# Kernel optimization log

Hardware: AMD Instinct MI355X
Metric: run time of the kernel (lower is better)

Reference implementation:

```python
import jax, jax.numpy as jnp
import numpy as np


def _lstm(x, w_ih, w_hh, b_ih, b_hh):
    # x: [B, T, D]; w_ih: [4H, D]; w_hh: [4H, H]. PyTorch gate order: i, f, g, o.
    B, T, D = x.shape
    H = w_hh.shape[1]
    # Precompute input contributions for all timesteps: [B, T, 4H]
    xg = jnp.einsum('btd,gd->btg', x, w_ih) + b_ih + b_hh
    xg = jnp.transpose(xg, (1, 0, 2))  # [T, B, 4H]

    def step(carry, xt):
        h, c = carry
        gates = xt + h @ w_hh.T  # [B, 4H]
        i, f, g, o = jnp.split(gates, 4, axis=-1)
        i = jax.nn.sigmoid(i)
        f = jax.nn.sigmoid(f)
        g = jnp.tanh(g)
        o = jax.nn.sigmoid(o)
        c = f * c + i * g
        h = o * jnp.tanh(c)
        return (h, c), h

    h0 = jnp.zeros((B, H), dtype=x.dtype)
    c0 = jnp.zeros((B, H), dtype=x.dtype)
    (_, _), hs = jax.lax.scan(step, (h0, c0), xg)
    return jnp.transpose(hs, (1, 0, 2))  # [B, T, H]


def setup_inputs() -> dict:
    key = jax.random.key(0)
    ks = jax.random.split(key, 11)
    B, T, D, H1, H2, OUT = 2048, 128, 128, 128, 64, 64
    s1 = 1.0 / np.sqrt(H1)
    s2 = 1.0 / np.sqrt(H2)
    return {
        'x': jax.random.normal(ks[0], (B, T, D), dtype=jnp.float32),
        'w_ih1': jax.random.uniform(ks[1], (4 * H1, D), jnp.float32, -s1, s1),
        'w_hh1': jax.random.uniform(ks[2], (4 * H1, H1), jnp.float32, -s1, s1),
        'b_ih1': jax.random.uniform(ks[3], (4 * H1,), jnp.float32, -s1, s1),
        'b_hh1': jax.random.uniform(ks[4], (4 * H1,), jnp.float32, -s1, s1),
        'w_ih2': jax.random.uniform(ks[5], (4 * H2, H1), jnp.float32, -s2, s2),
        'w_hh2': jax.random.uniform(ks[6], (4 * H2, H2), jnp.float32, -s2, s2),
        'b_ih2': jax.random.uniform(ks[7], (4 * H2,), jnp.float32, -s2, s2),
        'b_hh2': jax.random.uniform(ks[8], (4 * H2,), jnp.float32, -s2, s2),
        'w_dense': jax.random.uniform(ks[9], (OUT, H2), jnp.float32, -s2, s2),
        'b_dense': jax.random.uniform(ks[10], (OUT,), jnp.float32, -s2, s2),
    }


def reference(x, w_ih1, w_hh1, b_ih1, b_hh1, w_ih2, w_hh2, b_ih2, b_hh2, w_dense, b_dense):
    # Dropout is identity in eval mode.
    h = _lstm(x, w_ih1, w_hh1, b_ih1, b_hh1)          # [B, T, H1]
    h = _lstm(h, w_ih2, w_hh2, b_ih2, b_hh2)          # [B, T, H2]
    last = h[:, -1, :]                                 # [B, H2]
    return jax.nn.relu(last @ w_dense.T + b_dense)     # [B, 64]
```

## Files before the change

kernel.cpp:

```cpp
#include <hip/hip_runtime.h>
#include <hip/hip_bf16.h>

#define BB  2048
#define TT  128
#define DD  128
#define HH1 128
#define GG1 512
#define HH2 64
#define GG2 256
#define OO  64

typedef __attribute__((ext_vector_type(8))) short  short8;
typedef __attribute__((ext_vector_type(4))) float  floatx4;

#define PIN(x) asm volatile("" : "+v"(x))

#define OFF_WHH1 0
#define OFF_WIH1 131072
#define OFF_WIH2 262144
#define OFF_WHH2 327680
#define OFF_B1   360448
#define OFF_B2   362496
#define OFF_XBF  524288
#define OFF_H1S  67633152

__device__ __forceinline__ short f2bf(float f) {
  unsigned u = __float_as_uint(f);
  unsigned r = (u + 0x7FFFu + ((u >> 16) & 1u)) >> 16;
  return (short)r;
}
__device__ __forceinline__ float sigm(float x) {
  return __builtin_amdgcn_rcpf(1.0f + __expf(-x));
}
__device__ __forceinline__ float tanh_fast(float x) {
  return 1.0f - 2.0f * __builtin_amdgcn_rcpf(1.0f + __expf(2.0f * x));
}

__device__ __forceinline__ void lds_barrier() {
  asm volatile("s_waitcnt lgkmcnt(0)" ::: "memory");
  __builtin_amdgcn_s_barrier();
  asm volatile("" ::: "memory");
}

__global__ void k_prep(const float* __restrict__ wih1, const float* __restrict__ whh1,
                       const float* __restrict__ bih1, const float* __restrict__ bhh1,
                       const float* __restrict__ wih2, const float* __restrict__ whh2,
                       const float* __restrict__ bih2, const float* __restrict__ bhh2,
                       char* __restrict__ ws) {
  short* WHH1 = (short*)(ws + OFF_WHH1);
  short* WIH1 = (short*)(ws + OFF_WIH1);
  short* WIH2 = (short*)(ws + OFF_WIH2);
  short* WHH2 = (short*)(ws + OFF_WHH2);
  float* B1 = (float*)(ws + OFF_B1);
  float* B2 = (float*)(ws + OFF_B2);
  int idx = blockIdx.x * blockDim.x + threadIdx.x;
  int stride = gridDim.x * blockDim.x;
  for (int i = idx; i < GG1 * DD; i += stride) { WIH1[i] = f2bf(wih1[i]); WHH1[i] = f2bf(whh1[i]); }
  for (int i = idx; i < GG2 * HH1; i += stride) WIH2[i] = f2bf(wih2[i]);
  for (int i = idx; i < GG2 * HH2; i += stride) WHH2[i] = f2bf(whh2[i]);
  for (int i = idx; i < GG1; i += stride) B1[i] = bih1[i] + bhh1[i];
  for (int i = idx; i < GG2; i += stride) B2[i] = bih2[i] + bhh2[i];
}

__global__ __launch_bounds__(256) void k_xcast(const float* __restrict__ x,
                                               short* __restrict__ xbf) {
  size_t i = ((size_t)blockIdx.x * 256 + threadIdx.x) * 8;
  float4 a = *(const float4*)&x[i];
  float4 b = *(const float4*)&x[i + 4];
  short8 o;
  o[0] = f2bf(a.x); o[1] = f2bf(a.y); o[2] = f2bf(a.z); o[3] = f2bf(a.w);
  o[4] = f2bf(b.x); o[5] = f2bf(b.y); o[6] = f2bf(b.z); o[7] = f2bf(b.w);
  *(short8*)&xbf[i] = o;
}

__global__ __launch_bounds__(512, 2) void k_rec1f(const char* __restrict__ ws,
                                                  short* __restrict__ h1s) {
  __shared__ short hbds[2][16 * 136];
  const short* WHH = (const short*)(ws + OFF_WHH1);
  const short* WIH = (const short*)(ws + OFF_WIH1);
  const short* XBF = (const short*)(ws + OFF_XBF);
  const float* B1 = (const float*)(ws + OFF_B1);
  const int lane = threadIdx.x & 63;
  const int wv = threadIdx.x >> 6;
  const int col = lane & 15, quad = lane >> 4;
  const int hc = wv * 16 + col;
  const int r0 = blockIdx.x * 8;

  short8 wh[4][4], wx[4][4];
#pragma unroll
  for (int gt = 0; gt < 4; ++gt)
#pragma unroll
    for (int kk = 0; kk < 4; ++kk) {
      wh[gt][kk] = *(const short8*)&WHH[(gt * 128 + hc) * HH1 + kk * 32 + quad * 8];
      wx[gt][kk] = *(const short8*)&WIH[(gt * 128 + hc) * DD + kk * 32 + quad * 8];
      PIN(wh[gt][kk]);
      PIN(wx[gt][kk]);
    }
  float bias[4];
#pragma unroll
  for (int gt = 0; gt < 4; ++gt) bias[gt] = B1[gt * 128 + hc];

  for (int i = threadIdx.x; i < 2 * 16 * 136; i += 512) ((short*)hbds)[i] = 0;

  const bool aload = (col < 8);
  const short* xbase = XBF + (size_t)(r0 + (col & 7)) * TT * DD;
  const short8 zz = {0, 0, 0, 0, 0, 0, 0, 0};
  short8 ax_cur[4], ax_nxt[4];

  floatx4 accA[4], accB[4];
  {
    short8 ax0[4];
#pragma unroll
    for (int kk = 0; kk < 4; ++kk)
      ax0[kk] = aload ? *(const short8*)&xbase[kk * 32 + quad * 8] : zz;
#pragma unroll
    for (int gt = 0; gt < 4; ++gt)
      accA[gt] = (floatx4){bias[gt], bias[gt], bias[gt], bias[gt]};
#pragma unroll
    for (int kk = 0; kk < 4; ++kk)
#pragma unroll
      for (int gt = 0; gt < 4; ++gt)
        accA[gt] = __builtin_amdgcn_mfma_f32_16x16x32_bf16(ax0[kk], wx[gt][kk], accA[gt], 0, 0, 0);
  }
#pragma unroll
  for (int kk = 0; kk < 4; ++kk) {
    ax_cur[kk] = aload ? *(const short8*)&xbase[DD + kk * 32 + quad * 8] : zz;
    ax_nxt[kk] = ax_cur[kk];
  }

  const int row0 = (quad & 1) * 4 + (quad >> 1) * 2;
  float c0 = 0.f, c1 = 0.f;
  __syncthreads();

  auto step = [&](int t, short* rbuf, short* wbuf, floatx4* A, floatx4* Bn) {
    if (aload && t + 2 < TT) {
#pragma unroll
      for (int kk = 0; kk < 4; ++kk)
        ax_nxt[kk] = *(const short8*)&xbase[(t + 2) * DD + kk * 32 + quad * 8];
    }
    short8 ah[4];
#pragma unroll
    for (int kk = 0; kk < 4; ++kk)
      ah[kk] = *(const short8*)&rbuf[col * 136 + kk * 32 + quad * 8];
#pragma unroll
    for (int kk = 0; kk < 4; ++kk)
#pragma unroll
      for (int gt = 0; gt < 4; ++gt)
        A[gt] = __builtin_amdgcn_mfma_f32_16x16x32_bf16(ah[kk], wh[gt][kk], A[gt], 0, 0, 0);
#pragma unroll
    for (int gt = 0; gt < 4; ++gt)
      Bn[gt] = (floatx4){bias[gt], bias[gt], bias[gt], bias[gt]};
#pragma unroll
    for (int kk = 0; kk < 4; ++kk)
#pragma unroll
      for (int gt = 0; gt < 4; ++gt)
        Bn[gt] = __builtin_amdgcn_mfma_f32_16x16x32_bf16(ax_cur[kk], wx[gt][kk], Bn[gt], 0, 0, 0);

    float g0[4], g1[4];
#pragma unroll
    for (int gt = 0; gt < 4; ++gt) {
      float v2 = __shfl_xor(A[gt][2], 32);
      float v3 = __shfl_xor(A[gt][3], 32);
      g0[gt] = (quad < 2) ? A[gt][0] : v2;
      g1[gt] = (quad < 2) ? A[gt][1] : v3;
    }
    {
      float i0 = sigm(g0[0]), f0 = sigm(g0[1]), gg0 = tanh_fast(g0[2]), o0 = sigm(g0[3]);
      c0 = fmaf(f0, c0, i0 * gg0);
      float hA = o0 * tanh_fast(c0);
      float i1 = sigm(g1[0]), f1 = sigm(g1[1]), gg1 = tanh_fast(g1[2]), o1 = sigm(g1[3]);
      c1 = fmaf(f1, c1, i1 * gg1);
      float hB = o1 * tanh_fast(c1);
      short ha = f2bf(hA), hbv = f2bf(hB);
      wbuf[(row0)     * 136 + hc] = ha;
      wbuf[(row0 + 1) * 136 + hc] = hbv;
      h1s[((size_t)(r0 + row0)     * TT + t) * HH1 + hc] = ha;
      h1s[((size_t)(r0 + row0 + 1) * TT + t) * HH1 + hc] = hbv;
    }
    lds_barrier();
#pragma unroll
    for (int kk = 0; kk < 4; ++kk) ax_cur[kk] = ax_nxt[kk];
  };

  for (int t = 0; t < TT; t += 2) {
    step(t,     &hbds[0][0], &hbds[1][0], accA, accB);
    step(t + 1, &hbds[1][0], &hbds[0][0], accB, accA);
  }
}

__global__ __launch_bounds__(512, 2) void k_rec2f(const char* __restrict__ ws,
                                                  const short* __restrict__ h1s,
                                                  const float* __restrict__ wd,
                                                  const float* __restrict__ bd,
                                                  float* __restrict__ out) {
  __shared__ short hbuf[16 * 72];
  __shared__ float gsm[8 * 260];
  __shared__ float h2f[8 * HH2];
  const short* WHH = (const short*)(ws + OFF_WHH2);
  const short* WIH = (const short*)(ws + OFF_WIH2);
  const float* B2 = (const float*)(ws + OFF_B2);
  const int lane = threadIdx.x & 63;
  const int wv = threadIdx.x >> 6;
  const int col = lane & 15, quad = lane >> 4;
  const int n0 = wv * 32;
  const int r0 = blockIdx.x * 8;

  short8 wh[2][2], wx[2][4];
#pragma unroll
  for (int nt = 0; nt < 2; ++nt) {
#pragma unroll
    for (int kk = 0; kk < 2; ++kk) {
      wh[nt][kk] = *(const short8*)&WHH[(n0 + nt * 16 + col) * HH2 + kk * 32 + quad * 8];
      PIN(wh[nt][kk]);
    }
#pragma unroll
    for (int kk = 0; kk < 4; ++kk) {
      wx[nt][kk] = *(const short8*)&WIH[(n0 + nt * 16 + col) * HH1 + kk * 32 + quad * 8];
      PIN(wx[nt][kk]);
    }
  }
  float bias[2];
#pragma unroll
  for (int nt = 0; nt < 2; ++nt) bias[nt] = B2[n0 + nt * 16 + col];

  for (int i = threadIdx.x; i < 16 * 72; i += 512) hbuf[i] = 0;

  const bool aload = (col < 8);
  const short* h1base = h1s + (size_t)(r0 + (col & 7)) * TT * HH1;
  const short8 zz = {0, 0, 0, 0, 0, 0, 0, 0};
  short8 ax_cur[4], ax_nxt[4];

  floatx4 accA[2], accB[2];
  {
    short8 ax0[4];
#pragma unroll
    for (int kk = 0; kk < 4; ++kk)
      ax0[kk] = aload ? *(const short8*)&h1base[kk * 32 + quad * 8] : zz;
#pragma unroll
    for (int nt = 0; nt < 2; ++nt)
      accA[nt] = (floatx4){bias[nt], bias[nt], bias[nt], bias[nt]};
#pragma unroll
    for (int kk = 0; kk < 4; ++kk)
#pragma unroll
      for (int nt = 0; nt < 2; ++nt)
        accA[nt] = __builtin_amdgcn_mfma_f32_16x16x32_bf16(ax0[kk], wx[nt][kk], accA[nt], 0, 0, 0);
  }
#pragma unroll
  for (int kk = 0; kk < 4; ++kk) {
    ax_cur[kk] = aload ? *(const short8*)&h1base[HH1 + kk * 32 + quad * 8] : zz;
    ax_nxt[kk] = ax_cur[kk];
  }

  const int j = threadIdx.x & 63;
  const int rr = threadIdx.x >> 6;
  float cc = 0.f;
  __syncthreads();

  auto step = [&](int t, floatx4* A, floatx4* Bn) {
    short8 ah[2];
#pragma unroll
    for (int kk = 0; kk < 2; ++kk)
      ah[kk] = *(const short8*)&hbuf[col * 72 + kk * 32 + quad * 8];
#pragma unroll
    for (int kk = 0; kk < 2; ++kk)
#pragma unroll
      for (int nt = 0; nt < 2; ++nt)
        A[nt] = __builtin_amdgcn_mfma_f32_16x16x32_bf16(ah[kk], wh[nt][kk], A[nt], 0, 0, 0);

    if (quad < 2) {
#pragma unroll
      for (int nt = 0; nt < 2; ++nt)
#pragma unroll
        for (int r = 0; r < 4; ++r)
          gsm[(quad * 4 + r) * 260 + n0 + nt * 16 + col] = A[nt][r];
    }

#pragma unroll
    for (int nt = 0; nt < 2; ++nt)
      Bn[nt] = (floatx4){bias[nt], bias[nt], bias[nt], bias[nt]};
#pragma unroll
    for (int kk = 0; kk < 4; ++kk)
#pragma unroll
      for (int nt = 0; nt < 2; ++nt)
        Bn[nt] = __builtin_amdgcn_mfma_f32_16x16x32_bf16(ax_cur[kk], wx[nt][kk], Bn[nt], 0, 0, 0);
    if (aload && t + 2 < TT) {
#pragma unroll
      for (int kk = 0; kk < 4; ++kk)
        ax_nxt[kk] = *(const short8*)&h1base[(t + 2) * HH1 + kk * 32 + quad * 8];
    }

    lds_barrier();

    {
      float i0 = gsm[rr * 260 + j],       f0 = gsm[rr * 260 + 64 + j];
      float g0 = gsm[rr * 260 + 128 + j], o0 = gsm[rr * 260 + 192 + j];
      cc = fmaf(sigm(f0), cc, sigm(i0) * tanh_fast(g0));
      float hh = sigm(o0) * tanh_fast(cc);
      hbuf[rr * 72 + j] = f2bf(hh);
      if (t == TT - 1) h2f[rr * HH2 + j] = hh;
    }
    lds_barrier();
#pragma unroll
    for (int kk = 0; kk < 4; ++kk) ax_cur[kk] = ax_nxt[kk];
  };

  for (int t = 0; t < TT; t += 2) {
    step(t,     accA, accB);
    step(t + 1, accB, accA);
  }

  {
    const int o = threadIdx.x & 63;
    const int r = threadIdx.x >> 6;
    float acc = bd[o];
    for (int k = 0; k < HH2; ++k)
      acc = fmaf(h2f[r * HH2 + k], wd[o * HH2 + k], acc);
    out[(size_t)(r0 + r) * OO + o] = fmaxf(acc, 0.f);
  }
}

extern "C" void kernel_launch(void* const* d_in, const int* in_sizes, int n_in,
                              void* d_out, int out_size, void* d_ws, size_t ws_size,
                              hipStream_t stream) {
  const float* x       = (const float*)d_in[0];
  const float* w_ih1   = (const float*)d_in[1];
  const float* w_hh1   = (const float*)d_in[2];
  const float* b_ih1   = (const float*)d_in[3];
  const float* b_hh1   = (const float*)d_in[4];
  const float* w_ih2   = (const float*)d_in[5];
  const float* w_hh2   = (const float*)d_in[6];
  const float* b_ih2   = (const float*)d_in[7];
  const float* b_hh2   = (const float*)d_in[8];
  const float* w_dense = (const float*)d_in[9];
  const float* b_dense = (const float*)d_in[10];
  char* ws = (char*)d_ws;
  short* xbf = (short*)(ws + OFF_XBF);
  short* h1s = (short*)(ws + OFF_H1S);
  float* out = (float*)d_out;

  hipLaunchKernelGGL(k_prep, dim3(256), dim3(256), 0, stream,
                     w_ih1, w_hh1, b_ih1, b_hh1, w_ih2, w_hh2, b_ih2, b_hh2, ws);
  hipLaunchKernelGGL(k_xcast, dim3((BB * TT * DD) / (256 * 8)), dim3(256), 0, stream, x, xbf);
  hipLaunchKernelGGL(k_rec1f, dim3(BB / 8), dim3(512), 0, stream, ws, h1s);
  hipLaunchKernelGGL(k_rec2f, dim3(BB / 8), dim3(512), 0, stream, ws, h1s, w_dense, b_dense, out);
}
```

Measured before the change: 424.6 us.

## Prescale gate weights for exp2 activations and restructure layer-2 recurrence

```diff
diff --git a/kernel.cpp b/kernel.cpp
--- a/kernel.cpp
+++ b/kernel.cpp
@@ -24,16 +24,22 @@
 #define OFF_XBF  524288
 #define OFF_H1S  67633152
 
+#define L2E      1.44269504088896340736f
+#define TWO_L2E  2.88539008177792681472f
+
 __device__ __forceinline__ short f2bf(float f) {
   unsigned u = __float_as_uint(f);
   unsigned r = (u + 0x7FFFu + ((u >> 16) & 1u)) >> 16;
   return (short)r;
 }
-__device__ __forceinline__ float sigm(float x) {
-  return __builtin_amdgcn_rcpf(1.0f + __expf(-x));
-}
-__device__ __forceinline__ float tanh_fast(float x) {
-  return 1.0f - 2.0f * __builtin_amdgcn_rcpf(1.0f + __expf(2.0f * x));
+__device__ __forceinline__ float exp2_f(float x) {
+  float r; asm("v_exp_f32 %0, %1" : "=v"(r) : "v"(x)); return r;
+}
+__device__ __forceinline__ float sigm2(float y) {
+  return __builtin_amdgcn_rcpf(1.0f + exp2_f(y));
+}
+__device__ __forceinline__ float tanh2(float y) {
+  return fmaf(-2.0f, __builtin_amdgcn_rcpf(1.0f + exp2_f(y)), 1.0f);
 }
 
 __device__ __forceinline__ void lds_barrier() {
@@ -55,11 +61,28 @@
   float* B2 = (float*)(ws + OFF_B2);
   int idx = blockIdx.x * blockDim.x + threadIdx.x;
   int stride = gridDim.x * blockDim.x;
-  for (int i = idx; i < GG1 * DD; i += stride) { WIH1[i] = f2bf(wih1[i]); WHH1[i] = f2bf(whh1[i]); }
-  for (int i = idx; i < GG2 * HH1; i += stride) WIH2[i] = f2bf(wih2[i]);
-  for (int i = idx; i < GG2 * HH2; i += stride) WHH2[i] = f2bf(whh2[i]);
-  for (int i = idx; i < GG1; i += stride) B1[i] = bih1[i] + bhh1[i];
-  for (int i = idx; i < GG2; i += stride) B2[i] = bih2[i] + bhh2[i];
+  const float SCI = -L2E, SCG = TWO_L2E;
+  for (int i = idx; i < GG1 * DD; i += stride) {
+    int g = (i >> 7) >> 7;
+    float s = (g == 2) ? SCG : SCI;
+    WIH1[i] = f2bf(wih1[i] * s); WHH1[i] = f2bf(whh1[i] * s);
+  }
+  for (int i = idx; i < GG2 * HH1; i += stride) {
+    int g = (i >> 7) >> 6; float s = (g == 2) ? SCG : SCI;
+    WIH2[i] = f2bf(wih2[i] * s);
+  }
+  for (int i = idx; i < GG2 * HH2; i += stride) {
+    int g = (i >> 6) >> 6; float s = (g == 2) ? SCG : SCI;
+    WHH2[i] = f2bf(whh2[i] * s);
+  }
+  for (int i = idx; i < GG1; i += stride) {
+    float s = ((i >> 7) == 2) ? SCG : SCI;
+    B1[i] = (bih1[i] + bhh1[i]) * s;
+  }
+  for (int i = idx; i < GG2; i += stride) {
+    float s = ((i >> 6) == 2) ? SCG : SCI;
+    B2[i] = (bih2[i] + bhh2[i]) * s;
+  }
 }
 
 __global__ __launch_bounds__(256) void k_xcast(const float* __restrict__ x,
@@ -96,18 +119,22 @@
       PIN(wh[gt][kk]);
       PIN(wx[gt][kk]);
     }
-  float bias[4];
-#pragma unroll
-  for (int gt = 0; gt < 4; ++gt) bias[gt] = B1[gt * 128 + hc];
+  floatx4 BIASV[4];
+#pragma unroll
+  for (int gt = 0; gt < 4; ++gt) {
+    float b = B1[gt * 128 + hc];
+    BIASV[gt] = (floatx4){b, b, b, b};
+    PIN(BIASV[gt]);
+  }
 
   for (int i = threadIdx.x; i < 2 * 16 * 136; i += 512) ((short*)hbds)[i] = 0;
 
   const bool aload = (col < 8);
   const short* xbase = XBF + (size_t)(r0 + (col & 7)) * TT * DD;
   const short8 zz = {0, 0, 0, 0, 0, 0, 0, 0};
-  short8 ax_cur[4], ax_nxt[4];
-
+  short8 axA[4], axB[4];
   floatx4 accA[4], accB[4];
+
   {
     short8 ax0[4];
 #pragma unroll
@@ -115,28 +142,29 @@
       ax0[kk] = aload ? *(const short8*)&xbase[kk * 32 + quad * 8] : zz;
 #pragma unroll
     for (int gt = 0; gt < 4; ++gt)
-      accA[gt] = (floatx4){bias[gt], bias[gt], bias[gt], bias[gt]};
-#pragma unroll
-    for (int kk = 0; kk < 4; ++kk)
+      accA[gt] = __builtin_amdgcn_mfma_f32_16x16x32_bf16(ax0[0], wx[gt][0], BIASV[gt], 0, 0, 0);
+#pragma unroll
+    for (int kk = 1; kk < 4; ++kk)
 #pragma unroll
       for (int gt = 0; gt < 4; ++gt)
         accA[gt] = __builtin_amdgcn_mfma_f32_16x16x32_bf16(ax0[kk], wx[gt][kk], accA[gt], 0, 0, 0);
   }
 #pragma unroll
   for (int kk = 0; kk < 4; ++kk) {
-    ax_cur[kk] = aload ? *(const short8*)&xbase[DD + kk * 32 + quad * 8] : zz;
-    ax_nxt[kk] = ax_cur[kk];
+    axA[kk] = aload ? *(const short8*)&xbase[DD + kk * 32 + quad * 8] : zz;
+    axB[kk] = zz;
   }
 
   const int row0 = (quad & 1) * 4 + (quad >> 1) * 2;
   float c0 = 0.f, c1 = 0.f;
   __syncthreads();
 
-  auto step = [&](int t, short* rbuf, short* wbuf, floatx4* A, floatx4* Bn) {
+  auto step = [&](int t, short* rbuf, short* wbuf, floatx4* A, floatx4* Bn,
+                  short8* axC, short8* axP) {
     if (aload && t + 2 < TT) {
 #pragma unroll
       for (int kk = 0; kk < 4; ++kk)
-        ax_nxt[kk] = *(const short8*)&xbase[(t + 2) * DD + kk * 32 + quad * 8];
+        axP[kk] = *(const short8*)&xbase[(t + 2) * DD + kk * 32 + quad * 8];
     }
     short8 ah[4];
 #pragma unroll
@@ -149,12 +177,12 @@
         A[gt] = __builtin_amdgcn_mfma_f32_16x16x32_bf16(ah[kk], wh[gt][kk], A[gt], 0, 0, 0);
 #pragma unroll
     for (int gt = 0; gt < 4; ++gt)
-      Bn[gt] = (floatx4){bias[gt], bias[gt], bias[gt], bias[gt]};
-#pragma unroll
-    for (int kk = 0; kk < 4; ++kk)
-#pragma unroll
-      for (int gt = 0; gt < 4; ++gt)
-        Bn[gt] = __builtin_amdgcn_mfma_f32_16x16x32_bf16(ax_cur[kk], wx[gt][kk], Bn[gt], 0, 0, 0);
+      Bn[gt] = __builtin_amdgcn_mfma_f32_16x16x32_bf16(axC[0], wx[gt][0], BIASV[gt], 0, 0, 0);
+#pragma unroll
+    for (int kk = 1; kk < 4; ++kk)
+#pragma unroll
+      for (int gt = 0; gt < 4; ++gt)
+        Bn[gt] = __builtin_amdgcn_mfma_f32_16x16x32_bf16(axC[kk], wx[gt][kk], Bn[gt], 0, 0, 0);
 
     float g0[4], g1[4];
 #pragma unroll
@@ -165,12 +193,12 @@
       g1[gt] = (quad < 2) ? A[gt][1] : v3;
     }
     {
-      float i0 = sigm(g0[0]), f0 = sigm(g0[1]), gg0 = tanh_fast(g0[2]), o0 = sigm(g0[3]);
+      float i0 = sigm2(g0[0]), f0 = sigm2(g0[1]), gg0 = tanh2(g0[2]), o0 = sigm2(g0[3]);
       c0 = fmaf(f0, c0, i0 * gg0);
-      float hA = o0 * tanh_fast(c0);
-      float i1 = sigm(g1[0]), f1 = sigm(g1[1]), gg1 = tanh_fast(g1[2]), o1 = sigm(g1[3]);
+      float hA = o0 * tanh2(c0 * TWO_L2E);
+      float i1 = sigm2(g1[0]), f1 = sigm2(g1[1]), gg1 = tanh2(g1[2]), o1 = sigm2(g1[3]);
       c1 = fmaf(f1, c1, i1 * gg1);
-      float hB = o1 * tanh_fast(c1);
+      float hB = o1 * tanh2(c1 * TWO_L2E);
       short ha = f2bf(hA), hbv = f2bf(hB);
       wbuf[(row0)     * 136 + hc] = ha;
       wbuf[(row0 + 1) * 136 + hc] = hbv;
@@ -178,135 +206,140 @@
       h1s[((size_t)(r0 + row0 + 1) * TT + t) * HH1 + hc] = hbv;
     }
     lds_barrier();
-#pragma unroll
-    for (int kk = 0; kk < 4; ++kk) ax_cur[kk] = ax_nxt[kk];
   };
 
   for (int t = 0; t < TT; t += 2) {
-    step(t,     &hbds[0][0], &hbds[1][0], accA, accB);
-    step(t + 1, &hbds[1][0], &hbds[0][0], accB, accA);
-  }
-}
-
-__global__ __launch_bounds__(512, 2) void k_rec2f(const char* __restrict__ ws,
+    step(t,     &hbds[0][0], &hbds[1][0], accA, accB, axA, axB);
+    step(t + 1, &hbds[1][0], &hbds[0][0], accB, accA, axB, axA);
+  }
+}
+
+__global__ __launch_bounds__(256, 2) void k_rec2r(const char* __restrict__ ws,
                                                   const short* __restrict__ h1s,
                                                   const float* __restrict__ wd,
                                                   const float* __restrict__ bd,
                                                   float* __restrict__ out) {
-  __shared__ short hbuf[16 * 72];
-  __shared__ float gsm[8 * 260];
-  __shared__ float h2f[8 * HH2];
+  __shared__ short hbds[2][16 * 72];
+  __shared__ float h2f[4 * HH2];
   const short* WHH = (const short*)(ws + OFF_WHH2);
   const short* WIH = (const short*)(ws + OFF_WIH2);
   const float* B2 = (const float*)(ws + OFF_B2);
   const int lane = threadIdx.x & 63;
   const int wv = threadIdx.x >> 6;
   const int col = lane & 15, quad = lane >> 4;
-  const int n0 = wv * 32;
-  const int r0 = blockIdx.x * 8;
-
-  short8 wh[2][2], wx[2][4];
-#pragma unroll
-  for (int nt = 0; nt < 2; ++nt) {
+  const int hc = wv * 16 + col;
+  const int r0 = blockIdx.x * 4;
+
+  short8 wh[4][2], wx[4][4];
+#pragma unroll
+  for (int gt = 0; gt < 4; ++gt) {
 #pragma unroll
     for (int kk = 0; kk < 2; ++kk) {
-      wh[nt][kk] = *(const short8*)&WHH[(n0 + nt * 16 + col) * HH2 + kk * 32 + quad * 8];
-      PIN(wh[nt][kk]);
+      wh[gt][kk] = *(const short8*)&WHH[(gt * 64 + hc) * HH2 + kk * 32 + quad * 8];
+      PIN(wh[gt][kk]);
     }
 #pragma unroll
     for (int kk = 0; kk < 4; ++kk) {
-      wx[nt][kk] = *(const short8*)&WIH[(n0 + nt * 16 + col) * HH1 + kk * 32 + quad * 8];
-      PIN(wx[nt][kk]);
-    }
-  }
-  float bias[2];
-#pragma unroll
-  for (int nt = 0; nt < 2; ++nt) bias[nt] = B2[n0 + nt * 16 + col];
-
-  for (int i = threadIdx.x; i < 16 * 72; i += 512) hbuf[i] = 0;
-
-  const bool aload = (col < 8);
-  const short* h1base = h1s + (size_t)(r0 + (col & 7)) * TT * HH1;
+      wx[gt][kk] = *(const short8*)&WIH[(gt * 64 + hc) * HH1 + kk * 32 + quad * 8];
+      PIN(wx[gt][kk]);
+    }
+  }
+  floatx4 BIASV[4];
+#pragma unroll
+  for (int gt = 0; gt < 4; ++gt) {
+    float b = B2[gt * 64 + hc];
+    BIASV[gt] = (floatx4){b, b, b, b};
+    PIN(BIASV[gt]);
+  }
+
+  for (int i = threadIdx.x; i < 2 * 16 * 72; i += 256) ((short*)hbds)[i] = 0;
+
+  const bool aload = (col < 4);
+  const short* h1base = h1s + (size_t)(r0 + (col & 3)) * TT * HH1;
   const short8 zz = {0, 0, 0, 0, 0, 0, 0, 0};
-  short8 ax_cur[4], ax_nxt[4];
-
-  floatx4 accA[2], accB[2];
+  short8 axA[4], axB[4];
+  floatx4 accA[4], accB[4];
+
   {
     short8 ax0[4];
 #pragma unroll
     for (int kk = 0; kk < 4; ++kk)
       ax0[kk] = aload ? *(const short8*)&h1base[kk * 32 + quad * 8] : zz;
 #pragma unroll
-    for (int nt = 0; nt < 2; ++nt)
-      accA[nt] = (floatx4){bias[nt], bias[nt], bias[nt], bias[nt]};
-#pragma unroll
-    for (int kk = 0; kk < 4; ++kk)
-#pragma unroll
-      for (int nt = 0; nt < 2; ++nt)
-        accA[nt] = __builtin_amdgcn_mfma_f32_16x16x32_bf16(ax0[kk], wx[nt][kk], accA[nt], 0, 0, 0);
+    for (int gt = 0; gt < 4; ++gt)
+      accA[gt] = __builtin_amdgcn_mfma_f32_16x16x32_bf16(ax0[0], wx[gt][0], BIASV[gt], 0, 0, 0);
+#pragma unroll
+    for (int kk = 1; kk < 4; ++kk)
+#pragma unroll
+      for (int gt = 0; gt < 4; ++gt)
+        accA[gt] = __builtin_amdgcn_mfma_f32_16x16x32_bf16(ax0[kk], wx[gt][kk], accA[gt], 0, 0, 0);
   }
 #pragma unroll
   for (int kk = 0; kk < 4; ++kk) {
-    ax_cur[kk] = aload ? *(const short8*)&h1base[HH1 + kk * 32 + quad * 8] : zz;
-    ax_nxt[kk] = ax_cur[kk];
-  }
-
-  const int j = threadIdx.x & 63;
-  const int rr = threadIdx.x >> 6;
-  float cc = 0.f;
+    axA[kk] = aload ? *(const short8*)&h1base[HH1 + kk * 32 + quad * 8] : zz;
+    axB[kk] = zz;
+  }
+
+  const int row0 = (quad & 1) * 4 + (quad >> 1) * 2;
+  const bool realq = ((quad & 1) == 0);
+  float c0 = 0.f, c1 = 0.f;
   __syncthreads();
 
-  auto step = [&](int t, floatx4* A, floatx4* Bn) {
+  auto step = [&](int t, short* rbuf, short* wbuf, floatx4* A, floatx4* Bn,
+                  short8* axC, short8* axP) {
+    if (aload && t + 2 < TT) {
+#pragma unroll
+      for (int kk = 0; kk < 4; ++kk)
+        axP[kk] = *(const short8*)&h1base[(t + 2) * HH1 + kk * 32 + quad * 8];
+    }
     short8 ah[2];
 #pragma unroll
     for (int kk = 0; kk < 2; ++kk)
-      ah[kk] = *(const short8*)&hbuf[col * 72 + kk * 32 + quad * 8];
+      ah[kk] = *(const short8*)&rbuf[col * 72 + kk * 32 + quad * 8];
 #pragma unroll
     for (int kk = 0; kk < 2; ++kk)
 #pragma unroll
-      for (int nt = 0; nt < 2; ++nt)
-        A[nt] = __builtin_amdgcn_mfma_f32_16x16x32_bf16(ah[kk], wh[nt][kk], A[nt], 0, 0, 0);
-
-    if (quad < 2) {
-#pragma unroll
-      for (int nt = 0; nt < 2; ++nt)
-#pragma unroll
-        for (int r = 0; r < 4; ++r)
-          gsm[(quad * 4 + r) * 260 + n0 + nt * 16 + col] = A[nt][r];
-    }
-
-#pragma unroll
-    for (int nt = 0; nt < 2; ++nt)
-      Bn[nt] = (floatx4){bias[nt], bias[nt], bias[nt], bias[nt]};
-#pragma unroll
-    for (int kk = 0; kk < 4; ++kk)
-#pragma unroll
-      for (int nt = 0; nt < 2; ++nt)
-        Bn[nt] = __builtin_amdgcn_mfma_f32_16x16x32_bf16(ax_cur[kk], wx[nt][kk], Bn[nt], 0, 0, 0);
-    if (aload && t + 2 < TT) {
-#pragma unroll
-      for (int kk = 0; kk < 4; ++kk)
-        ax_nxt[kk] = *(const short8*)&h1base[(t + 2) * HH1 + kk * 32 + quad * 8];
-    }
-
+      for (int gt = 0; gt < 4; ++gt)
+        A[gt] = __builtin_amdgcn_mfma_f32_16x16x32_bf16(ah[kk], wh[gt][kk], A[gt], 0, 0, 0);
+#pragma unroll
+    for (int gt = 0; gt < 4; ++gt)
+      Bn[gt] = __builtin_amdgcn_mfma_f32_16x16x32_bf16(axC[0], wx[gt][0], BIASV[gt], 0, 0, 0);
+#pragma unroll
+    for (int kk = 1; kk < 4; ++kk)
+#pragma unroll
+      for (int gt = 0; gt < 4; ++gt)
+        Bn[gt] = __builtin_amdgcn_mfma_f32_16x16x32_bf16(axC[kk], wx[gt][kk], Bn[gt], 0, 0, 0);
+
+    float g0[4], g1[4];
+#pragma unroll
+    for (int gt = 0; gt < 4; ++gt) {
+      float v2 = __shfl_xor(A[gt][2], 32);
+      float v3 = __shfl_xor(A[gt][3], 32);
+      g0[gt] = (quad < 2) ? A[gt][0] : v2;
+      g1[gt] = (quad < 2) ? A[gt][1] : v3;
+    }
+    {
+      float i0 = sigm2(g0[0]), f0 = sigm2(g0[1]), gg0 = tanh2(g0[2]), o0 = sigm2(g0[3]);
+      c0 = fmaf(f0, c0, i0 * gg0);
+      float hA = o0 * tanh2(c0 * TWO_L2E);
+      float i1 = sigm2(g1[0]), f1 = sigm2(g1[1]), gg1 = tanh2(g1[2]), o1 = sigm2(g1[3]);
+      c1 = fmaf(f1, c1, i1 * gg1);
+      float hB = o1 * tanh2(c1 * TWO_L2E);
+      if (realq) {
+        wbuf[(row0)     * 72 + hc] = f2bf(hA);
+        wbuf[(row0 + 1) * 72 + hc] = f2bf(hB);
+        if (t == TT - 1) {
+          h2f[(row0)     * HH2 + hc] = hA;
+          h2f[(row0 + 1) * HH2 + hc] = hB;
+        }
+      }
+    }
     lds_barrier();
-
-    {
-      float i0 = gsm[rr * 260 + j],       f0 = gsm[rr * 260 + 64 + j];
-      float g0 = gsm[rr * 260 + 128 + j], o0 = gsm[rr * 260 + 192 + j];
-      cc = fmaf(sigm(f0), cc, sigm(i0) * tanh_fast(g0));
-      float hh = sigm(o0) * tanh_fast(cc);
-      hbuf[rr * 72 + j] = f2bf(hh);
-      if (t == TT - 1) h2f[rr * HH2 + j] = hh;
-    }
-    lds_barrier();
-#pragma unroll
-    for (int kk = 0; kk < 4; ++kk) ax_cur[kk] = ax_nxt[kk];
   };
 
   for (int t = 0; t < TT; t += 2) {
-    step(t,     accA, accB);
-    step(t + 1, accB, accA);
+    step(t,     &hbds[0][0], &hbds[1][0], accA, accB, axA, axB);
+    step(t + 1, &hbds[1][0], &hbds[0][0], accB, accA, axB, axA);
   }
 
   {
@@ -342,5 +375,5 @@
                      w_ih1, w_hh1, b_ih1, b_hh1, w_ih2, w_hh2, b_ih2, b_hh2, ws);
   hipLaunchKernelGGL(k_xcast, dim3((BB * TT * DD) / (256 * 8)), dim3(256), 0, stream, x, xbf);
   hipLaunchKernelGGL(k_rec1f, dim3(BB / 8), dim3(512), 0, stream, ws, h1s);
-  hipLaunchKernelGGL(k_rec2f, dim3(BB / 8), dim3(512), 0, stream, ws, h1s, w_dense, b_dense, out);
-}
+  hipLaunchKernelGGL(k_rec2r, dim3(BB / 4), dim3(256), 0, stream, ws, h1s, w_dense, b_dense, out);
+}
```

Measured after the change: 446.5 us. 1.05x slower.

## Fuse x bf16 cast into layer-1 recurrence and prescale gate weights for exp2

Applied to the files above, without the earlier changes.

```diff
diff --git a/kernel.cpp b/kernel.cpp
--- a/kernel.cpp
+++ b/kernel.cpp
@@ -21,19 +21,29 @@
 #define OFF_WHH2 327680
 #define OFF_B1   360448
 #define OFF_B2   362496
-#define OFF_XBF  524288
 #define OFF_H1S  67633152
+
+#define L2E      1.44269504088896340736f
+#define TWO_L2E  2.88539008177792681472f
 
 __device__ __forceinline__ short f2bf(float f) {
   unsigned u = __float_as_uint(f);
   unsigned r = (u + 0x7FFFu + ((u >> 16) & 1u)) >> 16;
   return (short)r;
 }
-__device__ __forceinline__ float sigm(float x) {
-  return __builtin_amdgcn_rcpf(1.0f + __expf(-x));
-}
-__device__ __forceinline__ float tanh_fast(float x) {
-  return 1.0f - 2.0f * __builtin_amdgcn_rcpf(1.0f + __expf(2.0f * x));
+__device__ __forceinline__ float exp2_f(float x) {
+  float r; asm("v_exp_f32 %0, %1" : "=v"(r) : "v"(x)); return r;
+}
+__device__ __forceinline__ float sigm2(float y) {
+  return __builtin_amdgcn_rcpf(1.0f + exp2_f(y));
+}
+__device__ __forceinline__ float tanh2(float y) {
+  return fmaf(-2.0f, __builtin_amdgcn_rcpf(1.0f + exp2_f(y)), 1.0f);
+}
+__device__ __forceinline__ unsigned cvtpk(float a, float b) {
+  unsigned r;
+  asm("v_cvt_pk_bf16_f32 %0, %1, %2" : "=v"(r) : "v"(a), "v"(b));
+  return r;
 }
 
 __device__ __forceinline__ void lds_barrier() {
@@ -55,30 +65,36 @@
   float* B2 = (float*)(ws + OFF_B2);
   int idx = blockIdx.x * blockDim.x + threadIdx.x;
   int stride = gridDim.x * blockDim.x;
-  for (int i = idx; i < GG1 * DD; i += stride) { WIH1[i] = f2bf(wih1[i]); WHH1[i] = f2bf(whh1[i]); }
-  for (int i = idx; i < GG2 * HH1; i += stride) WIH2[i] = f2bf(wih2[i]);
-  for (int i = idx; i < GG2 * HH2; i += stride) WHH2[i] = f2bf(whh2[i]);
-  for (int i = idx; i < GG1; i += stride) B1[i] = bih1[i] + bhh1[i];
-  for (int i = idx; i < GG2; i += stride) B2[i] = bih2[i] + bhh2[i];
-}
-
-__global__ __launch_bounds__(256) void k_xcast(const float* __restrict__ x,
-                                               short* __restrict__ xbf) {
-  size_t i = ((size_t)blockIdx.x * 256 + threadIdx.x) * 8;
-  float4 a = *(const float4*)&x[i];
-  float4 b = *(const float4*)&x[i + 4];
-  short8 o;
-  o[0] = f2bf(a.x); o[1] = f2bf(a.y); o[2] = f2bf(a.z); o[3] = f2bf(a.w);
-  o[4] = f2bf(b.x); o[5] = f2bf(b.y); o[6] = f2bf(b.z); o[7] = f2bf(b.w);
-  *(short8*)&xbf[i] = o;
+  const float SCI = -L2E, SCG = TWO_L2E;
+  for (int i = idx; i < GG1 * DD; i += stride) {
+    int g = (i >> 7) >> 7;
+    float s = (g == 2) ? SCG : SCI;
+    WIH1[i] = f2bf(wih1[i] * s); WHH1[i] = f2bf(whh1[i] * s);
+  }
+  for (int i = idx; i < GG2 * HH1; i += stride) {
+    int g = (i >> 7) >> 6; float s = (g == 2) ? SCG : SCI;
+    WIH2[i] = f2bf(wih2[i] * s);
+  }
+  for (int i = idx; i < GG2 * HH2; i += stride) {
+    int g = (i >> 6) >> 6; float s = (g == 2) ? SCG : SCI;
+    WHH2[i] = f2bf(whh2[i] * s);
+  }
+  for (int i = idx; i < GG1; i += stride) {
+    float s = ((i >> 7) == 2) ? SCG : SCI;
+    B1[i] = (bih1[i] + bhh1[i]) * s;
+  }
+  for (int i = idx; i < GG2; i += stride) {
+    float s = ((i >> 6) == 2) ? SCG : SCI;
+    B2[i] = (bih2[i] + bhh2[i]) * s;
+  }
 }
 
 __global__ __launch_bounds__(512, 2) void k_rec1f(const char* __restrict__ ws,
+                                                  const float* __restrict__ x,
                                                   short* __restrict__ h1s) {
   __shared__ short hbds[2][16 * 136];
   const short* WHH = (const short*)(ws + OFF_WHH1);
   const short* WIH = (const short*)(ws + OFF_WIH1);
-  const short* XBF = (const short*)(ws + OFF_XBF);
   const float* B1 = (const float*)(ws + OFF_B1);
   const int lane = threadIdx.x & 63;
   const int wv = threadIdx.x >> 6;
@@ -96,36 +112,48 @@
       PIN(wh[gt][kk]);
       PIN(wx[gt][kk]);
     }
-  float bias[4];
-#pragma unroll
-  for (int gt = 0; gt < 4; ++gt) bias[gt] = B1[gt * 128 + hc];
+  floatx4 BIASV[4];
+#pragma unroll
+  for (int gt = 0; gt < 4; ++gt) {
+    float b = B1[gt * 128 + hc];
+    BIASV[gt] = (floatx4){b, b, b, b};
+    PIN(BIASV[gt]);
+  }
 
   for (int i = threadIdx.x; i < 2 * 16 * 136; i += 512) ((short*)hbds)[i] = 0;
 
   const bool aload = (col < 8);
-  const short* xbase = XBF + (size_t)(r0 + (col & 7)) * TT * DD;
-  const short8 zz = {0, 0, 0, 0, 0, 0, 0, 0};
-  short8 ax_cur[4], ax_nxt[4];
+  const float* xbase = x + (size_t)(r0 + (col & 7)) * TT * DD;
+  float4 xf[4][2];
+#pragma unroll
+  for (int kk = 0; kk < 4; ++kk) {
+    xf[kk][0] = (float4){0.f, 0.f, 0.f, 0.f};
+    xf[kk][1] = (float4){0.f, 0.f, 0.f, 0.f};
+  }
 
   floatx4 accA[4], accB[4];
   {
     short8 ax0[4];
 #pragma unroll
-    for (int kk = 0; kk < 4; ++kk)
-      ax0[kk] = aload ? *(const short8*)&xbase[kk * 32 + quad * 8] : zz;
+    for (int kk = 0; kk < 4; ++kk) {
+      float4 f0 = (float4){0.f, 0.f, 0.f, 0.f}, f1 = f0;
+      if (aload) {
+        f0 = *(const float4*)&xbase[kk * 32 + quad * 8];
+        f1 = *(const float4*)&xbase[kk * 32 + quad * 8 + 4];
+      }
+      union { unsigned u[4]; short8 s; } cv;
+      cv.u[0] = cvtpk(f0.x, f0.y); cv.u[1] = cvtpk(f0.z, f0.w);
+      cv.u[2] = cvtpk(f1.x, f1.y); cv.u[3] = cvtpk(f1.z, f1.w);
+      ax0[kk] = cv.s;
+    }
 #pragma unroll
     for (int gt = 0; gt < 4; ++gt)
-      accA[gt] = (floatx4){bias[gt], bias[gt], bias[gt], bias[gt]};
-#pragma unroll
-    for (int kk = 0; kk < 4; ++kk)
+      accA[gt] = __builtin_amdgcn_mfma_f32_16x16x32_bf16(ax0[0], wx[gt][0], BIASV[gt], 0, 0, 0);
+#pragma unroll
+    for (int kk = 1; kk < 4; ++kk)
 #pragma unroll
       for (int gt = 0; gt < 4; ++gt)
         accA[gt] = __builtin_amdgcn_mfma_f32_16x16x32_bf16(ax0[kk], wx[gt][kk], accA[gt], 0, 0, 0);
-  }
-#pragma unroll
-  for (int kk = 0; kk < 4; ++kk) {
-    ax_cur[kk] = aload ? *(const short8*)&xbase[DD + kk * 32 + quad * 8] : zz;
-    ax_nxt[kk] = ax_cur[kk];
   }
 
   const int row0 = (quad & 1) * 4 + (quad >> 1) * 2;
@@ -133,10 +161,13 @@
   __syncthreads();
 
   auto step = [&](int t, short* rbuf, short* wbuf, floatx4* A, floatx4* Bn) {
-    if (aload && t + 2 < TT) {
-#pragma unroll
-      for (int kk = 0; kk < 4; ++kk)
-        ax_nxt[kk] = *(const short8*)&xbase[(t + 2) * DD + kk * 32 + quad * 8];
+    const bool doNext = (t + 1 < TT);
+    if (aload && doNext) {
+#pragma unroll
+      for (int kk = 0; kk < 4; ++kk) {
+        xf[kk][0] = *(const float4*)&xbase[(t + 1) * DD + kk * 32 + quad * 8];
+        xf[kk][1] = *(const float4*)&xbase[(t + 1) * DD + kk * 32 + quad * 8 + 4];
+      }
     }
     short8 ah[4];
 #pragma unroll
@@ -147,14 +178,26 @@
 #pragma unroll
       for (int gt = 0; gt < 4; ++gt)
         A[gt] = __builtin_amdgcn_mfma_f32_16x16x32_bf16(ah[kk], wh[gt][kk], A[gt], 0, 0, 0);
-#pragma unroll
-    for (int gt = 0; gt < 4; ++gt)
-      Bn[gt] = (floatx4){bias[gt], bias[gt], bias[gt], bias[gt]};
-#pragma unroll
-    for (int kk = 0; kk < 4; ++kk)
+    if (doNext) {
+      short8 axn[4];
+#pragma unroll
+      for (int kk = 0; kk < 4; ++kk) {
+        union { unsigned u[4]; short8 s; } cv;
+        cv.u[0] = cvtpk(xf[kk][0].x, xf[kk][0].y);
+        cv.u[1] = cvtpk(xf[kk][0].z, xf[kk][0].w);
+        cv.u[2] = cvtpk(xf[kk][1].x, xf[kk][1].y);
+        cv.u[3] = cvtpk(xf[kk][1].z, xf[kk][1].w);
+        axn[kk] = cv.s;
+      }
 #pragma unroll
       for (int gt = 0; gt < 4; ++gt)
-        Bn[gt] = __builtin_amdgcn_mfma_f32_16x16x32_bf16(ax_cur[kk], wx[gt][kk], Bn[gt], 0, 0, 0);
+        Bn[gt] = __builtin_amdgcn_mfma_f32_16x16x32_bf16(axn[0], wx[gt][0], BIASV[gt], 0, 0, 0);
+#pragma unroll
+      for (int kk = 1; kk < 4; ++kk)
+#pragma unroll
+        for (int gt = 0; gt < 4; ++gt)
+          Bn[gt] = __builtin_amdgcn_mfma_f32_16x16x32_bf16(axn[kk], wx[gt][kk], Bn[gt], 0, 0, 0);
+    }
 
     float g0[4], g1[4];
 #pragma unroll
@@ -165,12 +208,12 @@
       g1[gt] = (quad < 2) ? A[gt][1] : v3;
     }
     {
-      float i0 = sigm(g0[0]), f0 = sigm(g0[1]), gg0 = tanh_fast(g0[2]), o0 = sigm(g0[3]);
+      float i0 = sigm2(g0[0]), f0 = sigm2(g0[1]), gg0 = tanh2(g0[2]), o0 = sigm2(g0[3]);
       c0 = fmaf(f0, c0, i0 * gg0);
-      float hA = o0 * tanh_fast(c0);
-      float i1 = sigm(g1[0]), f1 = sigm(g1[1]), gg1 = tanh_fast(g1[2]), o1 = sigm(g1[3]);
+      float hA = o0 * tanh2(c0 * TWO_L2E);
+      float i1 = sigm2(g1[0]), f1 = sigm2(g1[1]), gg1 = tanh2(g1[2]), o1 = sigm2(g1[3]);
       c1 = fmaf(f1, c1, i1 * gg1);
-      float hB = o1 * tanh_fast(c1);
+      float hB = o1 * tanh2(c1 * TWO_L2E);
       short ha = f2bf(hA), hbv = f2bf(hB);
       wbuf[(row0)     * 136 + hc] = ha;
       wbuf[(row0 + 1) * 136 + hc] = hbv;
@@ -178,8 +221,6 @@
       h1s[((size_t)(r0 + row0 + 1) * TT + t) * HH1 + hc] = hbv;
     }
     lds_barrier();
-#pragma unroll
-    for (int kk = 0; kk < 4; ++kk) ax_cur[kk] = ax_nxt[kk];
   };
 
   for (int t = 0; t < TT; t += 2) {
@@ -219,18 +260,22 @@
       PIN(wx[nt][kk]);
     }
   }
-  float bias[2];
-#pragma unroll
-  for (int nt = 0; nt < 2; ++nt) bias[nt] = B2[n0 + nt * 16 + col];
+  floatx4 BIASV[2];
+#pragma unroll
+  for (int nt = 0; nt < 2; ++nt) {
+    float b = B2[n0 + nt * 16 + col];
+    BIASV[nt] = (floatx4){b, b, b, b};
+    PIN(BIASV[nt]);
+  }
 
   for (int i = threadIdx.x; i < 16 * 72; i += 512) hbuf[i] = 0;
 
   const bool aload = (col < 8);
   const short* h1base = h1s + (size_t)(r0 + (col & 7)) * TT * HH1;
   const short8 zz = {0, 0, 0, 0, 0, 0, 0, 0};
-  short8 ax_cur[4], ax_nxt[4];
-
+  short8 axA[4], axB[4];
   floatx4 accA[2], accB[2];
+
   {
     short8 ax0[4];
 #pragma unroll
@@ -238,17 +283,17 @@
       ax0[kk] = aload ? *(const short8*)&h1base[kk * 32 + quad * 8] : zz;
 #pragma unroll
     for (int nt = 0; nt < 2; ++nt)
-      accA[nt] = (floatx4){bias[nt], bias[nt], bias[nt], bias[nt]};
-#pragma unroll
-    for (int kk = 0; kk < 4; ++kk)
+      accA[nt] = __builtin_amdgcn_mfma_f32_16x16x32_bf16(ax0[0], wx[nt][0], BIASV[nt], 0, 0, 0);
+#pragma unroll
+    for (int kk = 1; kk < 4; ++kk)
 #pragma unroll
       for (int nt = 0; nt < 2; ++nt)
         accA[nt] = __builtin_amdgcn_mfma_f32_16x16x32_bf16(ax0[kk], wx[nt][kk], accA[nt], 0, 0, 0);
   }
 #pragma unroll
   for (int kk = 0; kk < 4; ++kk) {
-    ax_cur[kk] = aload ? *(const short8*)&h1base[HH1 + kk * 32 + quad * 8] : zz;
-    ax_nxt[kk] = ax_cur[kk];
+    axA[kk] = aload ? *(const short8*)&h1base[HH1 + kk * 32 + quad * 8] : zz;
+    axB[kk] = zz;
   }
 
   const int j = threadIdx.x & 63;
@@ -256,7 +301,7 @@
   float cc = 0.f;
   __syncthreads();
 
-  auto step = [&](int t, floatx4* A, floatx4* Bn) {
+  auto step = [&](int t, floatx4* A, floatx4* Bn, short8* axC, short8* axP) {
     short8 ah[2];
 #pragma unroll
     for (int kk = 0; kk < 2; ++kk)
@@ -277,16 +322,16 @@
 
 #pragma unroll
     for (int nt = 0; nt < 2; ++nt)
-      Bn[nt] = (floatx4){bias[nt], bias[nt], bias[nt], bias[nt]};
-#pragma unroll
-    for (int kk = 0; kk < 4; ++kk)
+      Bn[nt] = __builtin_amdgcn_mfma_f32_16x16x32_bf16(axC[0], wx[nt][0], BIASV[nt], 0, 0, 0);
+#pragma unroll
+    for (int kk = 1; kk < 4; ++kk)
 #pragma unroll
       for (int nt = 0; nt < 2; ++nt)
-        Bn[nt] = __builtin_amdgcn_mfma_f32_16x16x32_bf16(ax_cur[kk], wx[nt][kk], Bn[nt], 0, 0, 0);
+        Bn[nt] = __builtin_amdgcn_mfma_f32_16x16x32_bf16(axC[kk], wx[nt][kk], Bn[nt], 0, 0, 0);
     if (aload && t + 2 < TT) {
 #pragma unroll
       for (int kk = 0; kk < 4; ++kk)
-        ax_nxt[kk] = *(const short8*)&h1base[(t + 2) * HH1 + kk * 32 + quad * 8];
+        axP[kk] = *(const short8*)&h1base[(t + 2) * HH1 + kk * 32 + quad * 8];
     }
 
     lds_barrier();
@@ -294,19 +339,17 @@
     {
       float i0 = gsm[rr * 260 + j],       f0 = gsm[rr * 260 + 64 + j];
       float g0 = gsm[rr * 260 + 128 + j], o0 = gsm[rr * 260 + 192 + j];
-      cc = fmaf(sigm(f0), cc, sigm(i0) * tanh_fast(g0));
-      float hh = sigm(o0) * tanh_fast(cc);
+      cc = fmaf(sigm2(f0), cc, sigm2(i0) * tanh2(g0));
+      float hh = sigm2(o0) * tanh2(cc * TWO_L2E);
       hbuf[rr * 72 + j] = f2bf(hh);
       if (t == TT - 1) h2f[rr * HH2 + j] = hh;
     }
     lds_barrier();
-#pragma unroll
-    for (int kk = 0; kk < 4; ++kk) ax_cur[kk] = ax_nxt[kk];
   };
 
   for (int t = 0; t < TT; t += 2) {
-    step(t,     accA, accB);
-    step(t + 1, accB, accA);
+    step(t,     accA, accB, axA, axB);
+    step(t + 1, accB, accA, axB, axA);
   }
 
   {
@@ -334,13 +377,11 @@
   const float* w_dense = (const float*)d_in[9];
   const float* b_dense = (const float*)d_in[10];
   char* ws = (char*)d_ws;
-  short* xbf = (short*)(ws + OFF_XBF);
   short* h1s = (short*)(ws + OFF_H1S);
   float* out = (float*)d_out;
 
   hipLaunchKernelGGL(k_prep, dim3(256), dim3(256), 0, stream,
                      w_ih1, w_hh1, b_ih1, b_hh1, w_ih2, w_hh2, b_ih2, b_hh2, ws);
-  hipLaunchKernelGGL(k_xcast, dim3((BB * TT * DD) / (256 * 8)), dim3(256), 0, stream, x, xbf);
-  hipLaunchKernelGGL(k_rec1f, dim3(BB / 8), dim3(512), 0, stream, ws, h1s);
+  hipLaunchKernelGGL(k_rec1f, dim3(BB / 8), dim3(512), 0, stream, ws, x, h1s);
   hipLaunchKernelGGL(k_rec2f, dim3(BB / 8), dim3(512), 0, stream, ws, h1s, w_dense, b_dense, out);
 }
```

New measurement: 522.0 us. 1.23x slower.
